# Performance work log

Measured on AMD Instinct MI355X. Metric: run time of the kernel, lower is better.

The kernel has to match this reference:

```python
import jax, jax.numpy as jnp
import numpy as np

EPS = 1e-5

def _pairwise_sq_dist(x, e):
    # x: [N, D], e: [M, D] -> [N, M]; matches torch.addmm(||e||^2 + ||x||^2, x, e.T, alpha=-2, beta=1)
    return (jnp.sum(e * e, axis=1)[None, :]
            + jnp.sum(x * x, axis=1, keepdims=True)
            - 2.0 * (x @ e.T))

def _dist2ph(d, t):
    # softmax(-sqrt(d)/t); clamp tiny negative numerical residues before sqrt
    return jax.nn.softmax(-jnp.sqrt(jnp.maximum(d, 0.0)) / t, axis=-1)

def setup_inputs() -> dict:
    key = jax.random.key(0)
    k1, k2, k3 = jax.random.split(key, 3)
    B, T, D, M = 64, 128, 256, 1024
    audio_semantic = jax.random.normal(k1, (B, T, D), dtype=jnp.float32)
    video_semantic = jax.random.normal(k2, (B, T, D), dtype=jnp.float32)
    init_bound = 1.0 / 400.0
    embedding = jax.random.uniform(k3, (M, D), dtype=jnp.float32,
                                   minval=-init_bound, maxval=init_bound)
    return {"audio_semantic": audio_semantic,
            "video_semantic": video_semantic,
            "embedding": embedding}

def reference(audio_semantic, video_semantic, embedding):
    B, T, D = audio_semantic.shape
    M = embedding.shape[0]
    emb_sg = jax.lax.stop_gradient(embedding)

    # ---- VQ argmin + straight-through quantize (Audio/Video_vq_embedding) ----
    a_flat_sg = jax.lax.stop_gradient(audio_semantic).reshape(-1, D)
    v_flat_sg = jax.lax.stop_gradient(video_semantic).reshape(-1, D)
    a_idx = jnp.argmin(_pairwise_sq_dist(a_flat_sg, emb_sg), axis=-1)  # [B*T]
    v_idx = jnp.argmin(_pairwise_sq_dist(v_flat_sg, emb_sg), axis=-1)
    a_quantized = audio_semantic + jax.lax.stop_gradient(
        emb_sg[a_idx].reshape(B, T, D) - audio_semantic)
    v_quantized = video_semantic + jax.lax.stop_gradient(
        emb_sg[v_idx].reshape(B, T, D) - video_semantic)

    # ---- entropy-weighted cross-modal contrastive loss (cmcm_loss) ----
    a_dg = _pairwise_sq_dist(audio_semantic.reshape(-1, D), embedding)  # [B*T, M], grads flow
    v_dg = _pairwise_sq_dist(video_semantic.reshape(-1, D), embedding)

    a_pH = _dist2ph(a_dg, 1.0).reshape(B, T, M).transpose(1, 0, 2)     # [T, B, M]
    v_pH = _dist2ph(v_dg, 1.0).reshape(B, T, M).transpose(1, 0, 2)
    a_adj_ph = _dist2ph(a_dg, 0.5).reshape(B, T, M).transpose(1, 0, 2)
    v_adj_ph = _dist2ph(v_dg, 0.5).reshape(B, T, M).transpose(1, 0, 2)

    def cmcm(p_adj, q):
        # Scode[t] = p_adj[t] @ log(q[t]).T  -> [T, B, B]
        S = jnp.einsum('tbm,tcm->tbc', p_adj, jnp.log(q + 1e-10))
        S = S + jnp.max(-S)                 # matches MaxScode = max(-Scode)
        E = jnp.exp(S)
        diag = jnp.diagonal(E, axis1=-2, axis2=-1)          # [T, B]
        return -jnp.mean(jnp.log(diag / (jnp.sum(E, axis=-1) + EPS)))

    Lcmcm = cmcm(a_adj_ph, v_pH)
    Lcmcm2 = cmcm(v_adj_ph, a_pH)
    cmcm_loss = 0.5 * (Lcmcm + Lcmcm2)
    return cmcm_loss, a_quantized, v_quantized
```

## Files before the change

### kernel.cpp

```cpp
#include <hip/hip_runtime.h>

#define NROWS 8192
#define MCB   1024
#define DD    256
#define TT    128
#define BB    64

#define OFF_DA      0ul
#define OFF_DV      8388608ul
#define OFF_XX_A    16777216ul
#define OFF_XX_V    16785408ul
#define OFF_EE      16793600ul
#define OFF_SMIN_A  16794624ul
#define OFF_LZ1_A   16802816ul
#define OFF_IZ2_A   16811008ul
#define OFF_IDX_A   16819200ul
#define OFF_SMIN_V  16827392ul
#define OFF_LZ1_V   16835584ul
#define OFF_IZ2_V   16843776ul
#define OFF_IDX_V   16851968ul
#define OFF_S1      16860160ul
#define OFF_S2      17384448ul
#define OFF_PART    17908736ul
#define OFF_MAX     17908992ul
#define OFF_PACC    17909000ul
#define OFF_HIA     17909504ul
#define OFF_LOA     (OFF_HIA + 1048576ul)
#define OFF_HIV     (OFF_HIA + 2097152ul)
#define OFF_LOV     (OFF_HIA + 3145728ul)
#define OFF_HIE     (OFF_HIA + 4194304ul)
#define OFF_LOE     (OFF_HIE + 131072ul)

typedef __attribute__((ext_vector_type(8))) short bf16x8;
typedef __attribute__((ext_vector_type(4))) float f32x4;

__device__ __forceinline__ void gload_lds16u(const ushort* gsrc, ushort* ldst) {
  __builtin_amdgcn_global_load_lds(
      (const __attribute__((address_space(1))) void*)gsrc,
      (__attribute__((address_space(3))) void*)ldst, 16, 0, 0);
}
__device__ __forceinline__ ushort bf16_rne(float x) {
  unsigned u = __float_as_uint(x);
  unsigned r = u + 0x7FFFu + ((u >> 16) & 1u);
  return (ushort)(r >> 16);
}
__device__ __forceinline__ float bf16_f(ushort h) {
  return __uint_as_float((unsigned)h << 16);
}

__global__ void k_sumsq(const float* __restrict__ A, const float* __restrict__ V,
                        const float* __restrict__ E, float* __restrict__ ws) {
  const int lane = threadIdx.x & 63;
  const int wid  = threadIdx.x >> 6;
  const int row = blockIdx.x * 4 + wid;
  const float* src; float* dst; ushort* hi; ushort* lo; int r;
  if (row < 8192)       { src = A; r = row;         dst = ws + OFF_XX_A;
                          hi = (ushort*)(ws + OFF_HIA); lo = (ushort*)(ws + OFF_LOA); }
  else if (row < 16384) { src = V; r = row - 8192;  dst = ws + OFF_XX_V;
                          hi = (ushort*)(ws + OFF_HIV); lo = (ushort*)(ws + OFF_LOV); }
  else                  { src = E; r = row - 16384; dst = ws + OFF_EE;
                          hi = (ushort*)(ws + OFF_HIE); lo = (ushort*)(ws + OFF_LOE); }
  float4 x = *(const float4*)(src + (size_t)r * DD + lane * 4);
  ushort4 h, l;
  h.x = bf16_rne(x.x); l.x = bf16_rne(x.x - bf16_f(h.x));
  h.y = bf16_rne(x.y); l.y = bf16_rne(x.y - bf16_f(h.y));
  h.z = bf16_rne(x.z); l.z = bf16_rne(x.z - bf16_f(h.z));
  h.w = bf16_rne(x.w); l.w = bf16_rne(x.w - bf16_f(h.w));
  *(ushort4*)(hi + (size_t)r * DD + lane * 4) = h;
  *(ushort4*)(lo + (size_t)r * DD + lane * 4) = l;
  double acc = (double)x.x * x.x + (double)x.y * x.y +
               (double)x.z * x.z + (double)x.w * x.w;
  #pragma unroll
  for (int off = 32; off; off >>= 1) acc += __shfl_xor(acc, off);
  if (lane == 0) dst[r] = (float)acc;
}

__global__ __launch_bounds__(256) void k_dist(const float* __restrict__ A,
    const float* __restrict__ V, const float* __restrict__ E,
    float* __restrict__ ws) {
  const int z = blockIdx.z;
  const ushort* Xhi = (const ushort*)(ws + (z ? OFF_HIV : OFF_HIA));
  const ushort* Xlo = (const ushort*)(ws + (z ? OFF_LOV : OFF_LOA));
  const ushort* Ehi = (const ushort*)(ws + OFF_HIE);
  const ushort* Elo = (const ushort*)(ws + OFF_LOE);
  const float* xx = ws + (z ? OFF_XX_V : OFF_XX_A);
  const float* ee = ws + OFF_EE;
  float* Dst = ws + (z ? OFF_DV : OFF_DA);

  __shared__ __align__(16) ushort LAhi[128 * 32];
  __shared__ __align__(16) ushort LAlo[128 * 32];
  __shared__ __align__(16) ushort LBhi[128 * 32];
  __shared__ __align__(16) ushort LBlo[128 * 32];

  const int tid = threadIdx.x;
  const int bid = blockIdx.y * 8 + blockIdx.x;
  const int sw  = (bid & 7) * 64 + (bid >> 3);
  const int colb = sw & 7, rowb = sw >> 3;
  const int row0 = rowb * 128;
  const int col0 = colb * 128;

  const int wv = tid >> 6, lane = tid & 63;
  const int wr = wv >> 1, wc = wv & 1;
  const int rl = lane & 15, kg = lane >> 4;

  const int c0 = tid, c1 = 256 + tid;
  const int r0 = c0 >> 2, lg0 = (c0 & 3) ^ ((r0 >> 1) & 3);
  const int r1 = c1 >> 2, lg1 = (c1 & 3) ^ ((r1 >> 1) & 3);
  const ushort* gAhi0 = Xhi + (size_t)(row0 + r0) * DD + lg0 * 8;
  const ushort* gAhi1 = Xhi + (size_t)(row0 + r1) * DD + lg1 * 8;
  const ushort* gAlo0 = Xlo + (size_t)(row0 + r0) * DD + lg0 * 8;
  const ushort* gAlo1 = Xlo + (size_t)(row0 + r1) * DD + lg1 * 8;
  const ushort* gBhi0 = Ehi + (size_t)(col0 + r0) * DD + lg0 * 8;
  const ushort* gBhi1 = Ehi + (size_t)(col0 + r1) * DD + lg1 * 8;
  const ushort* gBlo0 = Elo + (size_t)(col0 + r0) * DD + lg0 * 8;
  const ushort* gBlo1 = Elo + (size_t)(col0 + r1) * DD + lg1 * 8;
  const int d0 = c0 * 8, d1 = c1 * 8;

  int aidx[4], bidx[4];
  #pragma unroll
  for (int f = 0; f < 4; ++f) {
    int ra = wr * 64 + f * 16 + rl;
    aidx[f] = ra * 32 + ((kg ^ ((ra >> 1) & 3)) << 3);
    int rb = wc * 64 + f * 16 + rl;
    bidx[f] = rb * 32 + ((kg ^ ((rb >> 1) & 3)) << 3);
  }

  f32x4 acc[4][4] = {};

  for (int t = 0; t < 8; ++t) {
    const int kc = t * 32;
    gload_lds16u(gAhi0 + kc, &LAhi[d0]);
    gload_lds16u(gAhi1 + kc, &LAhi[d1]);
    gload_lds16u(gAlo0 + kc, &LAlo[d0]);
    gload_lds16u(gAlo1 + kc, &LAlo[d1]);
    gload_lds16u(gBhi0 + kc, &LBhi[d0]);
    gload_lds16u(gBhi1 + kc, &LBhi[d1]);
    gload_lds16u(gBlo0 + kc, &LBlo[d0]);
    gload_lds16u(gBlo1 + kc, &LBlo[d1]);
    __syncthreads();
    __builtin_amdgcn_s_setprio(1);
    bf16x8 ahi[4], alo[4], bhi[4], blo[4];
    #pragma unroll
    for (int f = 0; f < 4; ++f) {
      ahi[f] = *(const bf16x8*)(&LAhi[aidx[f]]);
      alo[f] = *(const bf16x8*)(&LAlo[aidx[f]]);
      bhi[f] = *(const bf16x8*)(&LBhi[bidx[f]]);
      blo[f] = *(const bf16x8*)(&LBlo[bidx[f]]);
    }
    #pragma unroll
    for (int fr = 0; fr < 4; ++fr)
      #pragma unroll
      for (int fc = 0; fc < 4; ++fc) {
        acc[fr][fc] = __builtin_amdgcn_mfma_f32_16x16x32_bf16(
            ahi[fr], bhi[fc], acc[fr][fc], 0, 0, 0);
        acc[fr][fc] = __builtin_amdgcn_mfma_f32_16x16x32_bf16(
            ahi[fr], blo[fc], acc[fr][fc], 0, 0, 0);
        acc[fr][fc] = __builtin_amdgcn_mfma_f32_16x16x32_bf16(
            alo[fr], bhi[fc], acc[fr][fc], 0, 0, 0);
      }
    __builtin_amdgcn_s_setprio(0);
    __syncthreads();
  }

  float xn[4][4];
  #pragma unroll
  for (int fr = 0; fr < 4; ++fr)
    #pragma unroll
    for (int v = 0; v < 4; ++v)
      xn[fr][v] = xx[row0 + wr * 64 + fr * 16 + kg * 4 + v];
  #pragma unroll
  for (int fc = 0; fc < 4; ++fc) {
    const int m = col0 + wc * 64 + fc * 16 + rl;
    const float em = ee[m];
    #pragma unroll
    for (int fr = 0; fr < 4; ++fr) {
      #pragma unroll
      for (int v = 0; v < 4; ++v) {
        const int n = row0 + wr * 64 + fr * 16 + kg * 4 + v;
        Dst[(size_t)n * MCB + m] = (em + xn[fr][v]) - 2.0f * acc[fr][fc][v];
      }
    }
  }
}

__global__ void k_rowstats(const float* __restrict__ A, const float* __restrict__ V,
                           const float* __restrict__ E, float* __restrict__ ws,
                           float* __restrict__ out) {
  const int z = blockIdx.y;
  const float* Dm = ws + (z ? OFF_DV : OFF_DA);
  const float* X  = z ? V : A;
  float* smin_o = ws + (z ? OFF_SMIN_V : OFF_SMIN_A);
  float* lz1_o  = ws + (z ? OFF_LZ1_V  : OFF_LZ1_A);
  float* iz2_o  = ws + (z ? OFF_IZ2_V  : OFF_IZ2_A);
  int*   idx_o  = (int*)(ws + (z ? OFF_IDX_V : OFF_IDX_A));
  float* qout = out + 1 + (size_t)z * ((size_t)NROWS * DD);

  const int lane = threadIdx.x & 63, wid = threadIdx.x >> 6;
  const int n = blockIdx.x * 4 + wid;
  const float* drow = Dm + (size_t)n * MCB;

  float v[16];
  #pragma unroll
  for (int c = 0; c < 4; ++c) {
    float4 t = *(const float4*)(drow + c * 256 + lane * 4);
    v[c*4+0] = t.x; v[c*4+1] = t.y; v[c*4+2] = t.z; v[c*4+3] = t.w;
  }
  float bv = 3.4e38f; int bi = 0;
  #pragma unroll
  for (int c = 0; c < 4; ++c)
    #pragma unroll
    for (int j = 0; j < 4; ++j) {
      float val = v[c*4+j];
      int m = c * 256 + lane * 4 + j;
      if (val < bv) { bv = val; bi = m; }
    }
  #pragma unroll
  for (int off = 32; off; off >>= 1) {
    float ov = __shfl_xor(bv, off);
    int   oi = __shfl_xor(bi, off);
    if (ov < bv || (ov == bv && oi < bi)) { bv = ov; bi = oi; }
  }
  float smin = sqrtf(fmaxf(bv, 0.0f));
  float z1 = 0.f, z2 = 0.f;
  #pragma unroll
  for (int q = 0; q < 16; ++q) {
    float w = sqrtf(fmaxf(v[q], 0.0f)) - smin;
    z1 += __expf(-w);
    z2 += __expf(-2.0f * w);
  }
  #pragma unroll
  for (int off = 32; off; off >>= 1) {
    z1 += __shfl_xor(z1, off);
    z2 += __shfl_xor(z2, off);
  }
  if (lane == 0) {
    smin_o[n] = smin;
    lz1_o[n]  = __logf(z1);
    iz2_o[n]  = 1.0f / z2;
    idx_o[n]  = bi;
  }
  const float* erow = E + (size_t)bi * DD;
  const float* xrow = X + (size_t)n * DD;
  #pragma unroll
  for (int p = 0; p < 4; ++p) {
    int dd = p * 64 + lane;
    float xv = xrow[dd];
    float ev = erow[dd];
    qout[(size_t)n * DD + dd] = xv + (ev - xv);
  }
}

__global__ __launch_bounds__(512) void k_sgemm(float* __restrict__ ws) {
  const int z = blockIdx.y;
  const int t = blockIdx.x;
  const float* Dp = ws + (z ? OFF_DV : OFF_DA);
  const float* Dq = ws + (z ? OFF_DA : OFF_DV);
  const float* smin_p = ws + (z ? OFF_SMIN_V : OFF_SMIN_A);
  const float* iz2_p  = ws + (z ? OFF_IZ2_V  : OFF_IZ2_A);
  const float* smin_q = ws + (z ? OFF_SMIN_A : OFF_SMIN_V);
  const float* lz1_q  = ws + (z ? OFF_LZ1_A  : OFF_LZ1_V);
  float* S = ws + (z ? OFF_S2 : OFF_S1);
  float* part = ws + OFF_PART;

  __shared__ __align__(16) ushort PAs[2][64][32];
  __shared__ __align__(16) ushort WQs[2][64][32];
  __shared__ float sP[64], izP[64], sQ[64], lzQ[64];
  __shared__ float redmin[8];

  const int tid = threadIdx.x;
  const int wv = tid >> 6, lane = tid & 63;
  const int rl = lane & 15, kg = lane >> 4;
  const int bt  = (wv & 3) * 16;
  const int ctl = (wv >> 2) * 32;

  if (tid < 64) {
    size_t n = (size_t)tid * TT + t;
    sP[tid] = smin_p[n]; izP[tid] = iz2_p[n];
    sQ[tid] = smin_q[n]; lzQ[tid] = lz1_q[n];
  }
  __syncthreads();

  const int sb = tid >> 3;
  const int sm = (tid & 7) * 4;
  const float sPb = sP[sb], sQb = sQ[sb];
  const float* dpb = Dp + (size_t)(sb * TT + t) * MCB + sm;
  const float* dqb = Dq + (size_t)(sb * TT + t) * MCB + sm;

#define XF(rp, rq, buf) { \
    ushort4 hp, hq; \
    hp.x = bf16_rne(__expf(-2.f * (sqrtf(fmaxf((rp).x, 0.f)) - sPb))); \
    hp.y = bf16_rne(__expf(-2.f * (sqrtf(fmaxf((rp).y, 0.f)) - sPb))); \
    hp.z = bf16_rne(__expf(-2.f * (sqrtf(fmaxf((rp).z, 0.f)) - sPb))); \
    hp.w = bf16_rne(__expf(-2.f * (sqrtf(fmaxf((rp).w, 0.f)) - sPb))); \
    hq.x = bf16_rne(sqrtf(fmaxf((rq).x, 0.f)) - sQb); \
    hq.y = bf16_rne(sqrtf(fmaxf((rq).y, 0.f)) - sQb); \
    hq.z = bf16_rne(sqrtf(fmaxf((rq).z, 0.f)) - sQb); \
    hq.w = bf16_rne(sqrtf(fmaxf((rq).w, 0.f)) - sQb); \
    *(ushort4*)(&PAs[buf][sb][sm]) = hp; \
    *(ushort4*)(&WQs[buf][sb][sm]) = hq; }

#define MM(buf) { \
    bf16x8 af = *(const bf16x8*)(&PAs[buf][bt + rl][kg * 8]); \
    bf16x8 b0 = *(const bf16x8*)(&WQs[buf][ctl + rl][kg * 8]); \
    bf16x8 b1 = *(const bf16x8*)(&WQs[buf][ctl + 16 + rl][kg * 8]); \
    acc0 = __builtin_amdgcn_mfma_f32_16x16x32_bf16(af, b0, acc0, 0, 0, 0); \
    acc1 = __builtin_amdgcn_mfma_f32_16x16x32_bf16(af, b1, acc1, 0, 0, 0); }

  f32x4 acc0 = {}, acc1 = {};
  float4 rpA, rqA, rpB, rqB;

  rpA = *(const float4*)(dpb);        rqA = *(const float4*)(dqb);
  XF(rpA, rqA, 0)
  rpB = *(const float4*)(dpb + 32);   rqB = *(const float4*)(dqb + 32);

  #pragma unroll 4
  for (int c2 = 0; c2 < 16; ++c2) {
    const int che = c2 * 2;
    __syncthreads();
    if (che + 2 < 32) {
      rpA = *(const float4*)(dpb + (che + 2) * 32);
      rqA = *(const float4*)(dqb + (che + 2) * 32);
    }
    MM(0)
    XF(rpB, rqB, 1)
    __syncthreads();
    if (che + 3 < 32) {
      rpB = *(const float4*)(dpb + (che + 3) * 32);
      rqB = *(const float4*)(dqb + (che + 3) * 32);
    }
    MM(1)
    if (che + 2 < 32) XF(rpA, rqA, 0)
  }
#undef XF
#undef MM

  float mn = 3.4e38f;
  #pragma unroll
  for (int v = 0; v < 4; ++v) {
    const int b = bt + kg * 4 + v;
    const float izb = izP[b];
    float s0 = -izb * acc0[v] - lzQ[ctl + rl];
    float s1 = -izb * acc1[v] - lzQ[ctl + 16 + rl];
    S[((size_t)t * 64 + b) * 64 + ctl + rl]      = s0;
    S[((size_t)t * 64 + b) * 64 + ctl + 16 + rl] = s1;
    mn = fminf(mn, fminf(s0, s1));
  }
  #pragma unroll
  for (int off = 32; off; off >>= 1) mn = fminf(mn, __shfl_xor(mn, off));
  if (lane == 0) redmin[wv] = mn;
  __syncthreads();
  if (tid == 0) {
    float m = redmin[0];
    #pragma unroll
    for (int i = 1; i < 8; ++i) m = fminf(m, redmin[i]);
    part[z * 128 + t] = m;
  }
}

__global__ void k_sfinal(float* __restrict__ ws) {
  const float* part = ws + OFF_PART;
  float* maxv = ws + OFF_MAX;
  const int tens = threadIdx.x >> 7;
  const int i = threadIdx.x & 127;
  float m = part[tens * 128 + i];
  #pragma unroll
  for (int off = 32; off; off >>= 1) m = fminf(m, __shfl_xor(m, off));
  __shared__ float red[4];
  const int lane = threadIdx.x & 63, wid = threadIdx.x >> 6;
  if (lane == 0) red[wid] = m;
  __syncthreads();
  if (threadIdx.x == 0)   maxv[0] = -fminf(red[0], red[1]);
  if (threadIdx.x == 128) maxv[1] = -fminf(red[2], red[3]);
}

__global__ __launch_bounds__(256) void k_loss(float* __restrict__ ws) {
  const int lane = threadIdx.x & 63, wid = threadIdx.x >> 6;
  const int wglobal = blockIdx.x * 4 + wid;
  const float* Smax = ws + OFF_MAX;
  double acc = 0.0;
  #pragma unroll 4
  for (int r = 0; r < 16; ++r) {
    int gw = wglobal * 16 + r;
    int tens = gw >> 13;
    int rem = gw & 8191;
    const float* S = ws + (tens ? OFF_S2 : OFF_S1);
    float maxv = Smax[tens];
    float ev = __expf(S[(size_t)rem * 64 + lane] + maxv);
    float sum = ev;
    #pragma unroll
    for (int off = 32; off; off >>= 1) sum += __shfl_xor(sum, off);
    float diag = __shfl(ev, rem & 63);
    if (lane == 0) acc += (double)__logf(diag / (sum + 1e-5f));
  }
  __shared__ double red[4];
  if (lane == 0) red[wid] = acc;
  __syncthreads();
  if (threadIdx.x == 0)
    ((double*)(ws + OFF_PACC))[blockIdx.x] = red[0] + red[1] + red[2] + red[3];
}

__global__ void k_fin(const float* __restrict__ ws, float* __restrict__ out) {
  const double* p = (const double*)(ws + OFF_PACC);
  const int lane = threadIdx.x & 63, wid = threadIdx.x >> 6;
  double v = p[threadIdx.x];
  #pragma unroll
  for (int off = 32; off; off >>= 1) v += __shfl_xor(v, off);
  __shared__ double red[4];
  if (lane == 0) red[wid] = v;
  __syncthreads();
  if (threadIdx.x == 0)
    out[0] = (float)(-(red[0] + red[1] + red[2] + red[3]) / 16384.0);
}

extern "C" void kernel_launch(void* const* d_in, const int* in_sizes, int n_in,
                              void* d_out, int out_size, void* d_ws, size_t ws_size,
                              hipStream_t stream) {
  const float* A = (const float*)d_in[0];
  const float* V = (const float*)d_in[1];
  const float* E = (const float*)d_in[2];
  float* out = (float*)d_out;
  float* ws  = (float*)d_ws;

  k_sumsq  <<<dim3(4352), dim3(256), 0, stream>>>(A, V, E, ws);
  k_dist   <<<dim3(8, 64, 2), dim3(256), 0, stream>>>(A, V, E, ws);
  k_rowstats<<<dim3(2048, 2), dim3(256), 0, stream>>>(A, V, E, ws, out);
  k_sgemm  <<<dim3(128, 2), dim3(512), 0, stream>>>(ws);
  k_sfinal <<<dim3(1), dim3(256), 0, stream>>>(ws);
  k_loss   <<<dim3(256), dim3(256), 0, stream>>>(ws);
  k_fin    <<<dim3(1), dim3(256), 0, stream>>>(ws, out);
}
```

Measured before the change: 102.7 us.

## Precompute bf16 softmax operands in rowstats and stream them to LDS directly

The row-statistics kernel now computes the exp(-2w) and shifted-sqrt operands once per row and writes them as bf16 in place over the fp32 distance buffer. The contrastive GEMM kernel then loads these bf16 tiles directly into LDS with swizzled asynchronous global-to-LDS loads and double buffering. This removes the repeated sqrt/exp work and halves the bytes read by the GEMM. The cost is extra writes in rowstats and reliance on in-place reuse of the distance buffer.

```diff
diff --git a/kernel.cpp b/kernel.cpp
--- a/kernel.cpp
+++ b/kernel.cpp
@@ -187,7 +187,7 @@
                            const float* __restrict__ E, float* __restrict__ ws,
                            float* __restrict__ out) {
   const int z = blockIdx.y;
-  const float* Dm = ws + (z ? OFF_DV : OFF_DA);
+  float* Dm = ws + (z ? OFF_DV : OFF_DA);
   const float* X  = z ? V : A;
   float* smin_o = ws + (z ? OFF_SMIN_V : OFF_SMIN_A);
   float* lz1_o  = ws + (z ? OFF_LZ1_V  : OFF_LZ1_A);
@@ -197,7 +197,7 @@
 
   const int lane = threadIdx.x & 63, wid = threadIdx.x >> 6;
   const int n = blockIdx.x * 4 + wid;
-  const float* drow = Dm + (size_t)n * MCB;
+  float* drow = Dm + (size_t)n * MCB;
 
   float v[16];
   #pragma unroll
@@ -221,12 +221,14 @@
     if (ov < bv || (ov == bv && oi < bi)) { bv = ov; bi = oi; }
   }
   float smin = sqrtf(fmaxf(bv, 0.0f));
+  float w[16], e2[16];
   float z1 = 0.f, z2 = 0.f;
   #pragma unroll
   for (int q = 0; q < 16; ++q) {
-    float w = sqrtf(fmaxf(v[q], 0.0f)) - smin;
-    z1 += __expf(-w);
-    z2 += __expf(-2.0f * w);
+    w[q] = sqrtf(fmaxf(v[q], 0.0f)) - smin;
+    z1 += __expf(-w[q]);
+    e2[q] = __expf(-2.0f * w[q]);
+    z2 += e2[q];
   }
   #pragma unroll
   for (int off = 32; off; off >>= 1) {
@@ -239,6 +241,17 @@
     iz2_o[n]  = 1.0f / z2;
     idx_o[n]  = bi;
   }
+  ushort* prow = (ushort*)drow;
+  #pragma unroll
+  for (int c = 0; c < 4; ++c) {
+    ushort4 hp, hw;
+    hp.x = bf16_rne(e2[c*4+0]); hp.y = bf16_rne(e2[c*4+1]);
+    hp.z = bf16_rne(e2[c*4+2]); hp.w = bf16_rne(e2[c*4+3]);
+    hw.x = bf16_rne(w[c*4+0]);  hw.y = bf16_rne(w[c*4+1]);
+    hw.z = bf16_rne(w[c*4+2]);  hw.w = bf16_rne(w[c*4+3]);
+    *(ushort4*)(prow + c * 256 + lane * 4) = hp;
+    *(ushort4*)(prow + 1024 + c * 256 + lane * 4) = hw;
+  }
   const float* erow = E + (size_t)bi * DD;
   const float* xrow = X + (size_t)n * DD;
   #pragma unroll
@@ -253,18 +266,15 @@
 __global__ __launch_bounds__(512) void k_sgemm(float* __restrict__ ws) {
   const int z = blockIdx.y;
   const int t = blockIdx.x;
-  const float* Dp = ws + (z ? OFF_DV : OFF_DA);
-  const float* Dq = ws + (z ? OFF_DA : OFF_DV);
-  const float* smin_p = ws + (z ? OFF_SMIN_V : OFF_SMIN_A);
+  const ushort* P = (const ushort*)(ws + (z ? OFF_DV : OFF_DA));
+  const ushort* Q = (const ushort*)(ws + (z ? OFF_DA : OFF_DV));
   const float* iz2_p  = ws + (z ? OFF_IZ2_V  : OFF_IZ2_A);
-  const float* smin_q = ws + (z ? OFF_SMIN_A : OFF_SMIN_V);
   const float* lz1_q  = ws + (z ? OFF_LZ1_A  : OFF_LZ1_V);
   float* S = ws + (z ? OFF_S2 : OFF_S1);
   float* part = ws + OFF_PART;
 
-  __shared__ __align__(16) ushort PAs[2][64][32];
-  __shared__ __align__(16) ushort WQs[2][64][32];
-  __shared__ float sP[64], izP[64], sQ[64], lzQ[64];
+  __shared__ __align__(16) ushort PAs[2][64 * 64];
+  __shared__ __align__(16) ushort WQs[2][64 * 64];
   __shared__ float redmin[8];
 
   const int tid = threadIdx.x;
@@ -273,76 +283,59 @@
   const int bt  = (wv & 3) * 16;
   const int ctl = (wv >> 2) * 32;
 
-  if (tid < 64) {
-    size_t n = (size_t)tid * TT + t;
-    sP[tid] = smin_p[n]; izP[tid] = iz2_p[n];
-    sQ[tid] = smin_q[n]; lzQ[tid] = lz1_q[n];
-  }
+  const int sr = tid >> 3, sg = tid & 7;
+  const int lg = sg ^ (sr & 7);
+  const ushort* gP = P + (size_t)(sr * TT + t) * 2048 + lg * 8;
+  const ushort* gQ = Q + (size_t)(sr * TT + t) * 2048 + 1024 + lg * 8;
+  const int dso = tid * 8;
+
+  const int ra = bt + rl;
+  const int rb0 = ctl + rl, rb1 = ctl + 16 + rl;
+  int aoff[2], b0off[2], b1off[2];
+  #pragma unroll
+  for (int ks = 0; ks < 2; ++ks) {
+    int g = ks * 4 + kg;
+    aoff[ks]  = ra  * 64 + ((g ^ (ra  & 7)) * 8);
+    b0off[ks] = rb0 * 64 + ((g ^ (rb0 & 7)) * 8);
+    b1off[ks] = rb1 * 64 + ((g ^ (rb1 & 7)) * 8);
+  }
+
+  f32x4 acc0 = {}, acc1 = {};
+
+  gload_lds16u(gP, &PAs[0][dso]);
+  gload_lds16u(gQ, &WQs[0][dso]);
   __syncthreads();
 
-  const int sb = tid >> 3;
-  const int sm = (tid & 7) * 4;
-  const float sPb = sP[sb], sQb = sQ[sb];
-  const float* dpb = Dp + (size_t)(sb * TT + t) * MCB + sm;
-  const float* dqb = Dq + (size_t)(sb * TT + t) * MCB + sm;
-
-#define XF(rp, rq, buf) { \
-    ushort4 hp, hq; \
-    hp.x = bf16_rne(__expf(-2.f * (sqrtf(fmaxf((rp).x, 0.f)) - sPb))); \
-    hp.y = bf16_rne(__expf(-2.f * (sqrtf(fmaxf((rp).y, 0.f)) - sPb))); \
-    hp.z = bf16_rne(__expf(-2.f * (sqrtf(fmaxf((rp).z, 0.f)) - sPb))); \
-    hp.w = bf16_rne(__expf(-2.f * (sqrtf(fmaxf((rp).w, 0.f)) - sPb))); \
-    hq.x = bf16_rne(sqrtf(fmaxf((rq).x, 0.f)) - sQb); \
-    hq.y = bf16_rne(sqrtf(fmaxf((rq).y, 0.f)) - sQb); \
-    hq.z = bf16_rne(sqrtf(fmaxf((rq).z, 0.f)) - sQb); \
-    hq.w = bf16_rne(sqrtf(fmaxf((rq).w, 0.f)) - sQb); \
-    *(ushort4*)(&PAs[buf][sb][sm]) = hp; \
-    *(ushort4*)(&WQs[buf][sb][sm]) = hq; }
-
-#define MM(buf) { \
-    bf16x8 af = *(const bf16x8*)(&PAs[buf][bt + rl][kg * 8]); \
-    bf16x8 b0 = *(const bf16x8*)(&WQs[buf][ctl + rl][kg * 8]); \
-    bf16x8 b1 = *(const bf16x8*)(&WQs[buf][ctl + 16 + rl][kg * 8]); \
-    acc0 = __builtin_amdgcn_mfma_f32_16x16x32_bf16(af, b0, acc0, 0, 0, 0); \
-    acc1 = __builtin_amdgcn_mfma_f32_16x16x32_bf16(af, b1, acc1, 0, 0, 0); }
-
-  f32x4 acc0 = {}, acc1 = {};
-  float4 rpA, rqA, rpB, rqB;
-
-  rpA = *(const float4*)(dpb);        rqA = *(const float4*)(dqb);
-  XF(rpA, rqA, 0)
-  rpB = *(const float4*)(dpb + 32);   rqB = *(const float4*)(dqb + 32);
-
-  #pragma unroll 4
-  for (int c2 = 0; c2 < 16; ++c2) {
-    const int che = c2 * 2;
+  for (int ch = 0; ch < 16; ++ch) {
+    const int cur = ch & 1;
+    if (ch < 15) {
+      gload_lds16u(gP + (ch + 1) * 64, &PAs[cur ^ 1][dso]);
+      gload_lds16u(gQ + (ch + 1) * 64, &WQs[cur ^ 1][dso]);
+    }
+    __builtin_amdgcn_s_setprio(1);
+    #pragma unroll
+    for (int ks = 0; ks < 2; ++ks) {
+      bf16x8 af = *(const bf16x8*)(&PAs[cur][aoff[ks]]);
+      bf16x8 b0 = *(const bf16x8*)(&WQs[cur][b0off[ks]]);
+      bf16x8 b1 = *(const bf16x8*)(&WQs[cur][b1off[ks]]);
+      acc0 = __builtin_amdgcn_mfma_f32_16x16x32_bf16(af, b0, acc0, 0, 0, 0);
+      acc1 = __builtin_amdgcn_mfma_f32_16x16x32_bf16(af, b1, acc1, 0, 0, 0);
+    }
+    __builtin_amdgcn_s_setprio(0);
     __syncthreads();
-    if (che + 2 < 32) {
-      rpA = *(const float4*)(dpb + (che + 2) * 32);
-      rqA = *(const float4*)(dqb + (che + 2) * 32);
-    }
-    MM(0)
-    XF(rpB, rqB, 1)
-    __syncthreads();
-    if (che + 3 < 32) {
-      rpB = *(const float4*)(dpb + (che + 3) * 32);
-      rqB = *(const float4*)(dqb + (che + 3) * 32);
-    }
-    MM(1)
-    if (che + 2 < 32) XF(rpA, rqA, 0)
-  }
-#undef XF
-#undef MM
-
+  }
+
+  const float lzq0 = lz1_q[(size_t)rb0 * TT + t];
+  const float lzq1 = lz1_q[(size_t)rb1 * TT + t];
   float mn = 3.4e38f;
   #pragma unroll
   for (int v = 0; v < 4; ++v) {
     const int b = bt + kg * 4 + v;
-    const float izb = izP[b];
-    float s0 = -izb * acc0[v] - lzQ[ctl + rl];
-    float s1 = -izb * acc1[v] - lzQ[ctl + 16 + rl];
-    S[((size_t)t * 64 + b) * 64 + ctl + rl]      = s0;
-    S[((size_t)t * 64 + b) * 64 + ctl + 16 + rl] = s1;
+    const float izb = iz2_p[(size_t)b * TT + t];
+    float s0 = -izb * acc0[v] - lzq0;
+    float s1 = -izb * acc1[v] - lzq1;
+    S[((size_t)t * 64 + b) * 64 + rb0] = s0;
+    S[((size_t)t * 64 + b) * 64 + rb1] = s1;
     mn = fminf(mn, fminf(s0, s1));
   }
   #pragma unroll
```

Result: faster. 98.54 us (-4.0%).
